# Optimization experiments

Hardware: AMD Instinct MI355X
Metric: run time of the kernel (lower is better)

Reference implementation:

```python
import jax, jax.numpy as jnp
import numpy as np

SCALE_FLOOR = 0.001
N_SOURCES = 16


def setup_inputs() -> dict:
    key = jax.random.key(0)
    ks = jax.random.split(key, 8)
    n, d_in, d = 131072, 1024, 512
    x = jax.random.normal(ks[0], (n, d_in), dtype=jnp.float32)
    source_ids = jax.random.randint(ks[1], (n,), 0, N_SOURCES, dtype=jnp.int64)
    # backbone: single Linear(d_in -> d)
    Wb = jax.random.normal(ks[2], (d_in, d), dtype=jnp.float32) / np.sqrt(d_in)
    bb = jax.random.normal(ks[3], (d,), dtype=jnp.float32) * 0.01
    # pooled head: Linear(d -> 2)
    Wp = jax.random.normal(ks[4], (d, 2), dtype=jnp.float32) / np.sqrt(d)
    bp = jax.random.normal(ks[5], (2,), dtype=jnp.float32) * 0.01
    # per-source heads stacked: [S, d, 2], [S, 2]
    Ws = jax.random.normal(ks[6], (N_SOURCES, d, 2), dtype=jnp.float32) / np.sqrt(d)
    bs = jax.random.normal(ks[7], (N_SOURCES, 2), dtype=jnp.float32) * 0.01
    return {"x": x, "source_ids": source_ids, "Wb": Wb, "bb": bb,
            "Wp": Wp, "bp": bp, "Ws": Ws, "bs": bs}


def _head(raw):
    # raw: (n, 2) -> (mu, scale) with softplus + floor on scale
    mu = raw[:, 0]
    scale = jax.nn.softplus(raw[:, 1]) + SCALE_FLOOR
    return mu, scale


def reference(x, source_ids, Wb, bb, Wp, bp, Ws, bs):
    # backbone embedding: (n, d)
    emb = x @ Wb + bb
    # pooled head
    pooled_mu, pooled_scale = _head(emb @ Wp + bp)
    # routed per-source heads: compute all tiny heads, then gather per row.
    # raw_all: (n, S, 2); S*2 is tiny so this beats gather of per-row weights.
    raw_all = jnp.einsum('nd,sdk->nsk', emb, Ws) + bs[None, :, :]
    raw_sel = jnp.take_along_axis(raw_all, source_ids[:, None, None], axis=1)[:, 0, :]
    src_mu, src_scale = _head(raw_sel)
    # all source ids fall in [0, N_SOURCES), so every row is covered
    # (matches the torch loop where unmatched rows would stay zero).
    return emb, pooled_mu, pooled_scale, src_mu, src_scale
```

## Files before the change

### kernel.cpp

```cpp
#include <hip/hip_runtime.h>

typedef short bf16x8 __attribute__((ext_vector_type(8)));
typedef float f32x4 __attribute__((ext_vector_type(4)));

#define NROWS 131072L
#define DIN 1024
#define DEMB 512
#define NEXT 640

__device__ __forceinline__ unsigned short f2bf(float f) {
  unsigned u = __float_as_uint(f);
  u += 0x7FFFu + ((u >> 16) & 1u);
  return (unsigned short)(u >> 16);
}

__device__ __forceinline__ unsigned pkhi(float a, float b) {
  unsigned ua = __float_as_uint(a) + 0x8000u;
  unsigned ub = __float_as_uint(b) + 0x8000u;
  return __builtin_amdgcn_perm(ub, ua, 0x07060302u);
}

__device__ __forceinline__ float softplusf(float v) {
  return fmaxf(v, 0.f) + log1pf(expf(-fabsf(v)));
}

__global__ __launch_bounds__(256) void wb_transpose(const float* __restrict__ Wb,
                                                    unsigned short* __restrict__ WbT) {
  int g = blockIdx.x * 256 + threadIdx.x;
  int n = g & 511;
  int kb = g >> 9;
  unsigned short tmp[8];
#pragma unroll
  for (int j = 0; j < 8; ++j)
    tmp[j] = f2bf(Wb[(kb * 8 + j) * DEMB + n]);
  uint4 v;
  v.x = (unsigned)tmp[0] | ((unsigned)tmp[1] << 16);
  v.y = (unsigned)tmp[2] | ((unsigned)tmp[3] << 16);
  v.z = (unsigned)tmp[4] | ((unsigned)tmp[5] << 16);
  v.w = (unsigned)tmp[6] | ((unsigned)tmp[7] << 16);
  *(uint4*)(WbT + (long)n * DIN + kb * 8) = v;
}

__global__ void zero_tail(unsigned* __restrict__ p) {
  p[blockIdx.x * 256 + threadIdx.x] = 0u;
}

__global__ __launch_bounds__(256) void wfold_rows(const float* __restrict__ Wb,
                                                  const float* __restrict__ Wp,
                                                  const float* __restrict__ Ws,
                                                  unsigned short* __restrict__ WbT) {
  int w = threadIdx.x >> 6, lane = threadIdx.x & 63;
  int k = blockIdx.x * 4 + w;
  if (lane >= 34) return;
  const float* src;
  if (lane < 2) src = Wp + lane;
  else { int s = (lane - 2) >> 1; src = Ws + s * 1024 + (lane & 1); }
  const float* wrow = Wb + (long)k * DEMB;
  float acc = 0.f;
#pragma unroll 8
  for (int d = 0; d < DEMB; ++d) acc = fmaf(wrow[d], src[2 * d], acc);
  WbT[(long)(512 + lane) * DIN + k] = f2bf(acc);
}

__global__ void bfold_k(const float* __restrict__ bb, const float* __restrict__ Wp,
                        const float* __restrict__ bp, const float* __restrict__ Ws,
                        const float* __restrict__ bs, float* __restrict__ bf) {
  int j = threadIdx.x;
  if (j >= 34) return;
  const float* src; float bias;
  if (j < 2) { src = Wp + j; bias = bp[j]; }
  else { int s = (j - 2) >> 1; src = Ws + s * 1024 + (j & 1); bias = bs[s * 2 + (j & 1)]; }
  float acc = bias;
  for (int d = 0; d < DEMB; ++d) acc = fmaf(bb[d], src[2 * d], acc);
  bf[j] = acc;
}

__global__ __launch_bounds__(256, 3) void gemm_fused(
    const float* __restrict__ x, const unsigned short* __restrict__ wbt,
    const float* __restrict__ bb, const int* __restrict__ sid,
    const float* __restrict__ bfold, float* __restrict__ out) {
  __shared__ unsigned short SM[16384];
  unsigned short* const As0 = SM;
  unsigned short* const As1 = SM + 4096;
  unsigned short* const Bs0 = SM + 8192;
  unsigned short* const Bs1 = SM + 12288;

  const int t = threadIdx.x;
  const int lane = t & 63;
  const int wid = t >> 6;
  const int wm = wid >> 1, wn = wid & 1;

  const int bid = blockIdx.x;
  const int swz = (bid & 7) * 640 + (bid >> 3);
  const int mtile = swz / 5;
  const int ntile = swz - mtile * 5;
  const long m0 = (long)mtile * 128;
  const int n0 = ntile * 128;

  const int arow = t >> 3;
  const int akc = t & 7;
  const int abyte = arow * 64 + ((((akc >> 1) ^ ((t >> 4) & 3)) << 4)) + (akc & 1) * 8;
  const float* xbase = x + (m0 + arow) * DIN + akc * 4;

  const int bn = wid * 16 + (lane >> 2);
  const int bsg = (lane & 3) ^ ((lane >> 3) & 3);
  const unsigned short* bsrc = wbt + (long)(n0 + bn) * DIN + bsg * 8;

  const int l15 = lane & 15, lg = lane >> 4;
  const int kgo = ((lg ^ ((l15 >> 1) & 3)) << 4);
  const int ardrow = (wm * 64 + l15) * 64;
  const int brdrow = (wn * 64 + l15) * 64;

  f32x4 acc[4][4] = {};
  float4 aregA[4], aregB[4];

  auto loadA_A = [&](int k0) {
#pragma unroll
    for (int p = 0; p < 4; ++p)
      aregA[p] = *(const float4*)(xbase + (long)p * 32 * DIN + k0);
  };
  auto loadA_B = [&](int k0) {
#pragma unroll
    for (int p = 0; p < 4; ++p)
      aregB[p] = *(const float4*)(xbase + (long)p * 32 * DIN + k0);
  };
  auto stageB = [&](unsigned short* dst, int k0) {
#pragma unroll
    for (int i = 0; i < 2; ++i) {
      const unsigned short* gp = bsrc + (long)i * 64 * DIN + k0;
      unsigned short* lp = dst + (i * 256 + wid * 64) * 8;
      __builtin_amdgcn_global_load_lds(
          (const __attribute__((address_space(1))) void*)gp,
          (__attribute__((address_space(3))) void*)lp, 16, 0, 0);
    }
  };
  auto writeA_0A = [&]() {
    char* base = (char*)As0;
#pragma unroll
    for (int p = 0; p < 4; ++p) {
      uint2 v; v.x = pkhi(aregA[p].x, aregA[p].y); v.y = pkhi(aregA[p].z, aregA[p].w);
      *(uint2*)(base + abyte + p * 2048) = v;
    }
  };
  auto writeA_1B = [&]() {
    char* base = (char*)As1;
#pragma unroll
    for (int p = 0; p < 4; ++p) {
      uint2 v; v.x = pkhi(aregB[p].x, aregB[p].y); v.y = pkhi(aregB[p].z, aregB[p].w);
      *(uint2*)(base + abyte + p * 2048) = v;
    }
  };
  auto compute = [&](const unsigned short* Au, const unsigned short* Bu) {
    const char* Ab = (const char*)Au;
    const char* Bb = (const char*)Bu;
    bf16x8 af[4], bfv[4];
#pragma unroll
    for (int i = 0; i < 4; ++i) {
      af[i] = *(const bf16x8*)(Ab + ardrow + i * 1024 + kgo);
      bfv[i] = *(const bf16x8*)(Bb + brdrow + i * 1024 + kgo);
    }
#pragma unroll
    for (int mi = 0; mi < 4; ++mi)
#pragma unroll
      for (int ni = 0; ni < 4; ++ni)
        acc[mi][ni] = __builtin_amdgcn_mfma_f32_16x16x32_bf16(af[mi], bfv[ni],
                                                             acc[mi][ni], 0, 0, 0);
  };

  stageB(Bs0, 0);
  loadA_A(0);
  writeA_0A();
  loadA_B(32);
  __builtin_amdgcn_sched_barrier(0);
  asm volatile("s_waitcnt vmcnt(4) lgkmcnt(0)" ::: "memory");
  __builtin_amdgcn_sched_barrier(0);
  __builtin_amdgcn_s_barrier();

#pragma unroll 1
  for (int it = 0; it < 15; ++it) {
    const int ke = it * 2;
    stageB(Bs1, (ke + 1) * 32);
    __builtin_amdgcn_sched_barrier(0);
    loadA_A((ke + 2) * 32);
    compute(As0, Bs0);
    writeA_1B();
    __builtin_amdgcn_sched_barrier(0);
    asm volatile("s_waitcnt vmcnt(4) lgkmcnt(0)" ::: "memory");
    __builtin_amdgcn_sched_barrier(0);
    __builtin_amdgcn_s_barrier();
    stageB(Bs0, (ke + 2) * 32);
    __builtin_amdgcn_sched_barrier(0);
    loadA_B((ke + 3) * 32);
    compute(As1, Bs1);
    writeA_0A();
    __builtin_amdgcn_sched_barrier(0);
    asm volatile("s_waitcnt vmcnt(4) lgkmcnt(0)" ::: "memory");
    __builtin_amdgcn_sched_barrier(0);
    __builtin_amdgcn_s_barrier();
  }

  stageB(Bs1, 31 * 32);
  compute(As0, Bs0);
  writeA_1B();
  __builtin_amdgcn_sched_barrier(0);
  asm volatile("s_waitcnt vmcnt(0) lgkmcnt(0)" ::: "memory");
  __builtin_amdgcn_sched_barrier(0);
  __builtin_amdgcn_s_barrier();
  compute(As1, Bs1);

  if (ntile < 4) {
    const int colg = n0 + wn * 64 + l15;
    float bbv[4];
#pragma unroll
    for (int ni = 0; ni < 4; ++ni) bbv[ni] = bb[colg + ni * 16];
#pragma unroll
    for (int mi = 0; mi < 4; ++mi) {
      const long rbase = m0 + wm * 64 + mi * 16 + lg * 4;
#pragma unroll
      for (int ni = 0; ni < 4; ++ni)
#pragma unroll
        for (int r = 0; r < 4; ++r)
          out[(rbase + r) * DEMB + colg + ni * 16] = acc[mi][ni][r] + bbv[ni];
    }
  } else {
    __syncthreads();
    float* hl = (float*)SM;
    if (wn == 0) {
#pragma unroll
      for (int ni = 0; ni < 3; ++ni)
#pragma unroll
        for (int mi = 0; mi < 4; ++mi)
#pragma unroll
          for (int r = 0; r < 4; ++r) {
            int row = wm * 64 + mi * 16 + lg * 4 + r;
            hl[row * 49 + l15 + ni * 16] = acc[mi][ni][r];
          }
    }
    __syncthreads();
    if (t < 128) {
      const long row = m0 + t;
      const int s = sid[row];
      const float v0 = hl[t * 49 + 0] + bfold[0];
      const float v1 = hl[t * 49 + 1] + bfold[1];
      const float v2 = hl[t * 49 + 2 + 2 * s] + bfold[2 + 2 * s];
      const float v3 = hl[t * 49 + 3 + 2 * s] + bfold[3 + 2 * s];
      float* hp = out + NROWS * DEMB;
      hp[row] = v0;
      hp[NROWS + row] = softplusf(v1) + 0.001f;
      hp[2 * NROWS + row] = v2;
      hp[3 * NROWS + row] = softplusf(v3) + 0.001f;
    }
  }
}

extern "C" void kernel_launch(void* const* d_in, const int* in_sizes, int n_in,
                              void* d_out, int out_size, void* d_ws, size_t ws_size,
                              hipStream_t stream) {
  const float* x  = (const float*)d_in[0];
  const int* sid  = (const int*)d_in[1];
  const float* Wb = (const float*)d_in[2];
  const float* bb = (const float*)d_in[3];
  const float* Wp = (const float*)d_in[4];
  const float* bp = (const float*)d_in[5];
  const float* Ws = (const float*)d_in[6];
  const float* bs = (const float*)d_in[7];
  float* out = (float*)d_out;
  unsigned short* WbT = (unsigned short*)d_ws;
  float* bfoldp = (float*)(WbT + (long)NEXT * DIN);

  wb_transpose<<<256, 256, 0, stream>>>(Wb, WbT);
  zero_tail<<<188, 256, 0, stream>>>((unsigned*)(WbT + 546 * DIN));
  wfold_rows<<<256, 256, 0, stream>>>(Wb, Wp, Ws, WbT);
  bfold_k<<<1, 64, 0, stream>>>(bb, Wp, bp, Ws, bs, bfoldp);
  gemm_fused<<<5120, 256, 0, stream>>>(x, WbT, bb, sid, bfoldp, out);
}
```

Measured before the change: 360.5 us.

## Stream fp32 A tiles straight to LDS via async loads, convert at read

Reads of x no longer go through registers with a bf16 convert-and-store into LDS. fp32 A tiles are now loaded directly into LDS with global_load_lds into a triple-buffered, XOR-swizzled layout, and converted to bf16 when fragments are read for the MFMA. This removes the register staging and LDS write instructions and lets A prefetch run two stages ahead. In exchange LDS use grows to 64KB, launch bounds drop occupancy from 3 to 2 blocks, and each fragment read now needs twice the LDS reads plus pack instructions.

```diff
diff --git a/kernel.cpp b/kernel.cpp
--- a/kernel.cpp
+++ b/kernel.cpp
@@ -2,6 +2,7 @@
 
 typedef short bf16x8 __attribute__((ext_vector_type(8)));
 typedef float f32x4 __attribute__((ext_vector_type(4)));
+typedef unsigned uint4v __attribute__((ext_vector_type(4)));
 
 #define NROWS 131072L
 #define DIN 1024
@@ -75,15 +76,16 @@
   bf[j] = acc;
 }
 
-__global__ __launch_bounds__(256, 3) void gemm_fused(
+__global__ __launch_bounds__(256, 2) void gemm_fused(
     const float* __restrict__ x, const unsigned short* __restrict__ wbt,
     const float* __restrict__ bb, const int* __restrict__ sid,
     const float* __restrict__ bfold, float* __restrict__ out) {
-  __shared__ unsigned short SM[16384];
-  unsigned short* const As0 = SM;
-  unsigned short* const As1 = SM + 4096;
-  unsigned short* const Bs0 = SM + 8192;
-  unsigned short* const Bs1 = SM + 12288;
+  __shared__ __align__(16) char SM[65536];
+  char* const A0 = SM;
+  char* const A1 = SM + 16384;
+  char* const A2 = SM + 32768;
+  char* const B0 = SM + 49152;
+  char* const B1 = SM + 57344;
 
   const int t = threadIdx.x;
   const int lane = t & 63;
@@ -97,67 +99,53 @@
   const long m0 = (long)mtile * 128;
   const int n0 = ntile * 128;
 
-  const int arow = t >> 3;
-  const int akc = t & 7;
-  const int abyte = arow * 64 + ((((akc >> 1) ^ ((t >> 4) & 3)) << 4)) + (akc & 1) * 8;
-  const float* xbase = x + (m0 + arow) * DIN + akc * 4;
+  const int gswA = (t & 7) ^ ((t >> 3) & 7);
+  const float* xA = x + (m0 + (t >> 3)) * DIN + gswA * 4;
 
   const int bn = wid * 16 + (lane >> 2);
   const int bsg = (lane & 3) ^ ((lane >> 3) & 3);
   const unsigned short* bsrc = wbt + (long)(n0 + bn) * DIN + bsg * 8;
 
   const int l15 = lane & 15, lg = lane >> 4;
-  const int kgo = ((lg ^ ((l15 >> 1) & 3)) << 4);
-  const int ardrow = (wm * 64 + l15) * 64;
+  const int kgoB = ((lg ^ ((l15 >> 1) & 3)) << 4);
   const int brdrow = (wn * 64 + l15) * 64;
+  const int arow = (wm * 64 + l15) * 128;
+  const int g0x = (((lg * 2) ^ (l15 & 7)) << 4);
+  const int g1x = (((lg * 2 + 1) ^ (l15 & 7)) << 4);
 
   f32x4 acc[4][4] = {};
-  float4 aregA[4], aregB[4];
-
-  auto loadA_A = [&](int k0) {
-#pragma unroll
-    for (int p = 0; p < 4; ++p)
-      aregA[p] = *(const float4*)(xbase + (long)p * 32 * DIN + k0);
-  };
-  auto loadA_B = [&](int k0) {
-#pragma unroll
-    for (int p = 0; p < 4; ++p)
-      aregB[p] = *(const float4*)(xbase + (long)p * 32 * DIN + k0);
-  };
-  auto stageB = [&](unsigned short* dst, int k0) {
+
+  auto stageA = [&](char* Aw, int k0) {
+#pragma unroll
+    for (int p = 0; p < 4; ++p) {
+      const float* gp = xA + (long)p * 32 * DIN + k0;
+      __builtin_amdgcn_global_load_lds(
+          (const __attribute__((address_space(1))) void*)gp,
+          (__attribute__((address_space(3))) void*)(Aw + p * 4096 + wid * 1024),
+          16, 0, 0);
+    }
+  };
+  auto stageB = [&](char* Bw, int k0) {
 #pragma unroll
     for (int i = 0; i < 2; ++i) {
       const unsigned short* gp = bsrc + (long)i * 64 * DIN + k0;
-      unsigned short* lp = dst + (i * 256 + wid * 64) * 8;
       __builtin_amdgcn_global_load_lds(
           (const __attribute__((address_space(1))) void*)gp,
-          (__attribute__((address_space(3))) void*)lp, 16, 0, 0);
-    }
-  };
-  auto writeA_0A = [&]() {
-    char* base = (char*)As0;
-#pragma unroll
-    for (int p = 0; p < 4; ++p) {
-      uint2 v; v.x = pkhi(aregA[p].x, aregA[p].y); v.y = pkhi(aregA[p].z, aregA[p].w);
-      *(uint2*)(base + abyte + p * 2048) = v;
-    }
-  };
-  auto writeA_1B = [&]() {
-    char* base = (char*)As1;
-#pragma unroll
-    for (int p = 0; p < 4; ++p) {
-      uint2 v; v.x = pkhi(aregB[p].x, aregB[p].y); v.y = pkhi(aregB[p].z, aregB[p].w);
-      *(uint2*)(base + abyte + p * 2048) = v;
-    }
-  };
-  auto compute = [&](const unsigned short* Au, const unsigned short* Bu) {
-    const char* Ab = (const char*)Au;
-    const char* Bb = (const char*)Bu;
+          (__attribute__((address_space(3))) void*)(Bw + i * 4096 + wid * 1024),
+          16, 0, 0);
+    }
+  };
+  auto compute = [&](const char* Ac, const char* Bc) {
     bf16x8 af[4], bfv[4];
 #pragma unroll
     for (int i = 0; i < 4; ++i) {
-      af[i] = *(const bf16x8*)(Ab + ardrow + i * 1024 + kgo);
-      bfv[i] = *(const bf16x8*)(Bb + brdrow + i * 1024 + kgo);
+      f32x4 q0 = *(const f32x4*)(Ac + arow + i * 2048 + g0x);
+      f32x4 q1 = *(const f32x4*)(Ac + arow + i * 2048 + g1x);
+      uint4v u;
+      u[0] = pkhi(q0[0], q0[1]); u[1] = pkhi(q0[2], q0[3]);
+      u[2] = pkhi(q1[0], q1[1]); u[3] = pkhi(q1[2], q1[3]);
+      af[i] = __builtin_bit_cast(bf16x8, u);
+      bfv[i] = *(const bf16x8*)(Bc + brdrow + i * 1024 + kgoB);
     }
 #pragma unroll
     for (int mi = 0; mi < 4; ++mi)
@@ -166,47 +154,40 @@
         acc[mi][ni] = __builtin_amdgcn_mfma_f32_16x16x32_bf16(af[mi], bfv[ni],
                                                              acc[mi][ni], 0, 0, 0);
   };
-
-  stageB(Bs0, 0);
-  loadA_A(0);
-  writeA_0A();
-  loadA_B(32);
-  __builtin_amdgcn_sched_barrier(0);
-  asm volatile("s_waitcnt vmcnt(4) lgkmcnt(0)" ::: "memory");
-  __builtin_amdgcn_sched_barrier(0);
-  __builtin_amdgcn_s_barrier();
-
-#pragma unroll 1
-  for (int it = 0; it < 15; ++it) {
-    const int ke = it * 2;
-    stageB(Bs1, (ke + 1) * 32);
-    __builtin_amdgcn_sched_barrier(0);
-    loadA_A((ke + 2) * 32);
-    compute(As0, Bs0);
-    writeA_1B();
+  auto body = [&](char* Ac, char* Aw, char* Bc, char* Bw, int tt) {
+    stageB(Bw, (tt + 1) * 32);
+    stageA(Aw, (tt + 2) * 32);
+    compute(Ac, Bc);
     __builtin_amdgcn_sched_barrier(0);
     asm volatile("s_waitcnt vmcnt(4) lgkmcnt(0)" ::: "memory");
     __builtin_amdgcn_sched_barrier(0);
     __builtin_amdgcn_s_barrier();
-    stageB(Bs0, (ke + 2) * 32);
-    __builtin_amdgcn_sched_barrier(0);
-    loadA_B((ke + 3) * 32);
-    compute(As1, Bs1);
-    writeA_0A();
-    __builtin_amdgcn_sched_barrier(0);
-    asm volatile("s_waitcnt vmcnt(4) lgkmcnt(0)" ::: "memory");
-    __builtin_amdgcn_sched_barrier(0);
-    __builtin_amdgcn_s_barrier();
+  };
+
+  stageA(A0, 0);
+  stageB(B0, 0);
+  stageA(A1, 32);
+  __builtin_amdgcn_sched_barrier(0);
+  asm volatile("s_waitcnt vmcnt(4) lgkmcnt(0)" ::: "memory");
+  __builtin_amdgcn_sched_barrier(0);
+  __builtin_amdgcn_s_barrier();
+
+#pragma unroll 1
+  for (int tb = 0; tb < 30; tb += 6) {
+    body(A0, A2, B0, B1, tb + 0);
+    body(A1, A0, B1, B0, tb + 1);
+    body(A2, A1, B0, B1, tb + 2);
+    body(A0, A2, B1, B0, tb + 3);
+    body(A1, A0, B0, B1, tb + 4);
+    body(A2, A1, B1, B0, tb + 5);
   }
-
-  stageB(Bs1, 31 * 32);
-  compute(As0, Bs0);
-  writeA_1B();
+  stageB(B1, 31 * 32);
+  compute(A0, B0);
   __builtin_amdgcn_sched_barrier(0);
   asm volatile("s_waitcnt vmcnt(0) lgkmcnt(0)" ::: "memory");
   __builtin_amdgcn_sched_barrier(0);
   __builtin_amdgcn_s_barrier();
-  compute(As1, Bs1);
+  compute(A1, B1);
 
   if (ntile < 4) {
     const int colg = n0 + wn * 64 + l15;
```

New measurement: 366.2 us. About the same (+1.6%).

## Shrink GEMM N-tile to 64 columns to cut padded head work and raise occupancy

Applied to the files above, without the earlier changes.

The fused GEMM tile changes from 128x128 to 128x64. The grid becomes 9 column tiles per row block: 8 for the embedding and 1 for the 34 folded head columns, replacing 5 tiles covering 640 padded columns. This cuts wasted MFMA work on the padded head columns, halves accumulator registers and allows 4 blocks per CU. In exchange, each x row tile is loaded and converted to bf16 nine times instead of five, so activation traffic and conversion VALU work rise. The head epilogue is rewritten for the narrower tile with a 35-float LDS stride.

```diff
diff --git a/kernel.cpp b/kernel.cpp
--- a/kernel.cpp
+++ b/kernel.cpp
@@ -75,15 +75,15 @@
   bf[j] = acc;
 }
 
-__global__ __launch_bounds__(256, 3) void gemm_fused(
+__global__ __launch_bounds__(256, 4) void gemm_fused(
     const float* __restrict__ x, const unsigned short* __restrict__ wbt,
     const float* __restrict__ bb, const int* __restrict__ sid,
     const float* __restrict__ bfold, float* __restrict__ out) {
-  __shared__ unsigned short SM[16384];
-  unsigned short* const As0 = SM;
-  unsigned short* const As1 = SM + 4096;
-  unsigned short* const Bs0 = SM + 8192;
-  unsigned short* const Bs1 = SM + 12288;
+  __shared__ __align__(16) char SM[24576];
+  char* const As0 = SM;
+  char* const As1 = SM + 8192;
+  char* const B0  = SM + 16384;
+  char* const B1  = SM + 20480;
 
   const int t = threadIdx.x;
   const int lane = t & 63;
@@ -91,27 +91,25 @@
   const int wm = wid >> 1, wn = wid & 1;
 
   const int bid = blockIdx.x;
-  const int swz = (bid & 7) * 640 + (bid >> 3);
-  const int mtile = swz / 5;
-  const int ntile = swz - mtile * 5;
+  const int swz = (bid & 7) * 1152 + (bid >> 3);
+  const int mtile = swz / 9;
+  const int ntile = swz - mtile * 9;
   const long m0 = (long)mtile * 128;
-  const int n0 = ntile * 128;
-
-  const int arow = t >> 3;
+  const int n0 = ntile * 64;
+
   const int akc = t & 7;
-  const int abyte = arow * 64 + ((((akc >> 1) ^ ((t >> 4) & 3)) << 4)) + (akc & 1) * 8;
-  const float* xbase = x + (m0 + arow) * DIN + akc * 4;
-
-  const int bn = wid * 16 + (lane >> 2);
-  const int bsg = (lane & 3) ^ ((lane >> 3) & 3);
-  const unsigned short* bsrc = wbt + (long)(n0 + bn) * DIN + bsg * 8;
+  const int abyte = (t >> 3) * 64 + ((((akc >> 1) ^ ((t >> 4) & 3)) << 4)) + (akc & 1) * 8;
+  const float* xbase = x + (m0 + (t >> 3)) * DIN + akc * 4;
+
+  const unsigned short* bsrc =
+      wbt + (long)(n0 + (t >> 2)) * DIN + ((t & 3) ^ ((t >> 3) & 3)) * 8;
 
   const int l15 = lane & 15, lg = lane >> 4;
   const int kgo = ((lg ^ ((l15 >> 1) & 3)) << 4);
   const int ardrow = (wm * 64 + l15) * 64;
-  const int brdrow = (wn * 64 + l15) * 64;
-
-  f32x4 acc[4][4] = {};
+  const int brdrow = (wn * 32 + l15) * 64;
+
+  f32x4 acc[4][2] = {};
   float4 aregA[4], aregB[4];
 
   auto loadA_A = [&](int k0) {
@@ -124,18 +122,15 @@
     for (int p = 0; p < 4; ++p)
       aregB[p] = *(const float4*)(xbase + (long)p * 32 * DIN + k0);
   };
-  auto stageB = [&](unsigned short* dst, int k0) {
-#pragma unroll
-    for (int i = 0; i < 2; ++i) {
-      const unsigned short* gp = bsrc + (long)i * 64 * DIN + k0;
-      unsigned short* lp = dst + (i * 256 + wid * 64) * 8;
-      __builtin_amdgcn_global_load_lds(
-          (const __attribute__((address_space(1))) void*)gp,
-          (__attribute__((address_space(3))) void*)lp, 16, 0, 0);
-    }
+  auto stageB = [&](char* Bw, int k0) {
+    const unsigned short* gp = bsrc + k0;
+    __builtin_amdgcn_global_load_lds(
+        (const __attribute__((address_space(1))) void*)gp,
+        (__attribute__((address_space(3))) void*)(Bw + wid * 1024),
+        16, 0, 0);
   };
   auto writeA_0A = [&]() {
-    char* base = (char*)As0;
+    char* base = As0;
 #pragma unroll
     for (int p = 0; p < 4; ++p) {
       uint2 v; v.x = pkhi(aregA[p].x, aregA[p].y); v.y = pkhi(aregA[p].z, aregA[p].w);
@@ -143,31 +138,30 @@
     }
   };
   auto writeA_1B = [&]() {
-    char* base = (char*)As1;
+    char* base = As1;
 #pragma unroll
     for (int p = 0; p < 4; ++p) {
       uint2 v; v.x = pkhi(aregB[p].x, aregB[p].y); v.y = pkhi(aregB[p].z, aregB[p].w);
       *(uint2*)(base + abyte + p * 2048) = v;
     }
   };
-  auto compute = [&](const unsigned short* Au, const unsigned short* Bu) {
-    const char* Ab = (const char*)Au;
-    const char* Bb = (const char*)Bu;
-    bf16x8 af[4], bfv[4];
-#pragma unroll
-    for (int i = 0; i < 4; ++i) {
+  auto compute = [&](const char* Ab, const char* Bb) {
+    bf16x8 af[4], bfv[2];
+#pragma unroll
+    for (int i = 0; i < 4; ++i)
       af[i] = *(const bf16x8*)(Ab + ardrow + i * 1024 + kgo);
+#pragma unroll
+    for (int i = 0; i < 2; ++i)
       bfv[i] = *(const bf16x8*)(Bb + brdrow + i * 1024 + kgo);
-    }
 #pragma unroll
     for (int mi = 0; mi < 4; ++mi)
 #pragma unroll
-      for (int ni = 0; ni < 4; ++ni)
+      for (int ni = 0; ni < 2; ++ni)
         acc[mi][ni] = __builtin_amdgcn_mfma_f32_16x16x32_bf16(af[mi], bfv[ni],
                                                              acc[mi][ni], 0, 0, 0);
   };
 
-  stageB(Bs0, 0);
+  stageB(B0, 0);
   loadA_A(0);
   writeA_0A();
   loadA_B(32);
@@ -177,47 +171,43 @@
   __builtin_amdgcn_s_barrier();
 
 #pragma unroll 1
-  for (int it = 0; it < 15; ++it) {
-    const int ke = it * 2;
-    stageB(Bs1, (ke + 1) * 32);
-    __builtin_amdgcn_sched_barrier(0);
-    loadA_A((ke + 2) * 32);
-    compute(As0, Bs0);
+  for (int tb = 0; tb < 30; tb += 2) {
+    stageB(B1, (tb + 1) * 32);
+    loadA_A((tb + 2) * 32);
+    compute(As0, B0);
     writeA_1B();
     __builtin_amdgcn_sched_barrier(0);
     asm volatile("s_waitcnt vmcnt(4) lgkmcnt(0)" ::: "memory");
     __builtin_amdgcn_sched_barrier(0);
     __builtin_amdgcn_s_barrier();
-    stageB(Bs0, (ke + 2) * 32);
-    __builtin_amdgcn_sched_barrier(0);
-    loadA_B((ke + 3) * 32);
-    compute(As1, Bs1);
+    stageB(B0, (tb + 2) * 32);
+    loadA_B((tb + 3) * 32);
+    compute(As1, B1);
     writeA_0A();
     __builtin_amdgcn_sched_barrier(0);
     asm volatile("s_waitcnt vmcnt(4) lgkmcnt(0)" ::: "memory");
     __builtin_amdgcn_sched_barrier(0);
     __builtin_amdgcn_s_barrier();
   }
-
-  stageB(Bs1, 31 * 32);
-  compute(As0, Bs0);
+  stageB(B1, 31 * 32);
+  compute(As0, B0);
   writeA_1B();
   __builtin_amdgcn_sched_barrier(0);
   asm volatile("s_waitcnt vmcnt(0) lgkmcnt(0)" ::: "memory");
   __builtin_amdgcn_sched_barrier(0);
   __builtin_amdgcn_s_barrier();
-  compute(As1, Bs1);
-
-  if (ntile < 4) {
-    const int colg = n0 + wn * 64 + l15;
-    float bbv[4];
-#pragma unroll
-    for (int ni = 0; ni < 4; ++ni) bbv[ni] = bb[colg + ni * 16];
+  compute(As1, B1);
+
+  if (ntile < 8) {
+    const int colg = n0 + wn * 32 + l15;
+    float bbv[2];
+#pragma unroll
+    for (int ni = 0; ni < 2; ++ni) bbv[ni] = bb[colg + ni * 16];
 #pragma unroll
     for (int mi = 0; mi < 4; ++mi) {
       const long rbase = m0 + wm * 64 + mi * 16 + lg * 4;
 #pragma unroll
-      for (int ni = 0; ni < 4; ++ni)
+      for (int ni = 0; ni < 2; ++ni)
 #pragma unroll
         for (int r = 0; r < 4; ++r)
           out[(rbase + r) * DEMB + colg + ni * 16] = acc[mi][ni][r] + bbv[ni];
@@ -225,25 +215,29 @@
   } else {
     __syncthreads();
     float* hl = (float*)SM;
-    if (wn == 0) {
-#pragma unroll
-      for (int ni = 0; ni < 3; ++ni)
-#pragma unroll
-        for (int mi = 0; mi < 4; ++mi)
-#pragma unroll
-          for (int r = 0; r < 4; ++r) {
-            int row = wm * 64 + mi * 16 + lg * 4 + r;
-            hl[row * 49 + l15 + ni * 16] = acc[mi][ni][r];
-          }
+    if (wn == 0 || (wn == 1 && l15 < 2)) {
+#pragma unroll
+      for (int ni = 0; ni < 2; ++ni) {
+        int col = wn * 32 + ni * 16 + l15;
+        if (col < 34) {
+#pragma unroll
+          for (int mi = 0; mi < 4; ++mi)
+#pragma unroll
+            for (int r = 0; r < 4; ++r) {
+              int row = wm * 64 + mi * 16 + lg * 4 + r;
+              hl[row * 35 + col] = acc[mi][ni][r];
+            }
+        }
+      }
     }
     __syncthreads();
     if (t < 128) {
       const long row = m0 + t;
       const int s = sid[row];
-      const float v0 = hl[t * 49 + 0] + bfold[0];
-      const float v1 = hl[t * 49 + 1] + bfold[1];
-      const float v2 = hl[t * 49 + 2 + 2 * s] + bfold[2 + 2 * s];
-      const float v3 = hl[t * 49 + 3 + 2 * s] + bfold[3 + 2 * s];
+      const float v0 = hl[t * 35 + 0] + bfold[0];
+      const float v1 = hl[t * 35 + 1] + bfold[1];
+      const float v2 = hl[t * 35 + 2 + 2 * s] + bfold[2 + 2 * s];
+      const float v3 = hl[t * 35 + 3 + 2 * s] + bfold[3 + 2 * s];
       float* hp = out + NROWS * DEMB;
       hp[row] = v0;
       hp[NROWS + row] = softplusf(v1) + 0.001f;
@@ -272,5 +266,5 @@
   zero_tail<<<188, 256, 0, stream>>>((unsigned*)(WbT + 546 * DIN));
   wfold_rows<<<256, 256, 0, stream>>>(Wb, Wp, Ws, WbT);
   bfold_k<<<1, 64, 0, stream>>>(bb, Wp, bp, Ws, bs, bfoldp);
-  gemm_fused<<<5120, 256, 0, stream>>>(x, WbT, bb, sid, bfoldp, out);
-}
+  gemm_fused<<<9216, 256, 0, stream>>>(x, WbT, bb, sid, bfoldp, out);
+}
```

Result: slower. 406.8 us (+12.8%).

## Triple-buffer B tiles with two-deep prefetch and raise MFMA wave priority

Applied to the files above, without the earlier changes.

The GEMM main loop moves from double-buffered B (weight) tiles to three LDS B buffers, so weight tiles are staged two K-steps ahead while x loads stay one step ahead in registers. The loop is unrolled six phases per iteration through a macro, and the waitcnt threshold is relaxed to allow more loads in flight. s_setprio is raised around the MFMA block to favour compute issue. This is meant to hide global-load latency better, at the cost of 40KB of LDS per block instead of 32KB, which may reduce occupancy.

```diff
diff --git a/kernel.cpp b/kernel.cpp
--- a/kernel.cpp
+++ b/kernel.cpp
@@ -79,11 +79,12 @@
     const float* __restrict__ x, const unsigned short* __restrict__ wbt,
     const float* __restrict__ bb, const int* __restrict__ sid,
     const float* __restrict__ bfold, float* __restrict__ out) {
-  __shared__ unsigned short SM[16384];
-  unsigned short* const As0 = SM;
-  unsigned short* const As1 = SM + 4096;
-  unsigned short* const Bs0 = SM + 8192;
-  unsigned short* const Bs1 = SM + 12288;
+  __shared__ __align__(16) char SM[40960];
+  char* const As0 = SM;
+  char* const As1 = SM + 8192;
+  char* const B0  = SM + 16384;
+  char* const B1  = SM + 24576;
+  char* const B2  = SM + 32768;
 
   const int t = threadIdx.x;
   const int lane = t & 63;
@@ -97,10 +98,9 @@
   const long m0 = (long)mtile * 128;
   const int n0 = ntile * 128;
 
-  const int arow = t >> 3;
   const int akc = t & 7;
-  const int abyte = arow * 64 + ((((akc >> 1) ^ ((t >> 4) & 3)) << 4)) + (akc & 1) * 8;
-  const float* xbase = x + (m0 + arow) * DIN + akc * 4;
+  const int abyte = (t >> 3) * 64 + ((((akc >> 1) ^ ((t >> 4) & 3)) << 4)) + (akc & 1) * 8;
+  const float* xbase = x + (m0 + (t >> 3)) * DIN + akc * 4;
 
   const int bn = wid * 16 + (lane >> 2);
   const int bsg = (lane & 3) ^ ((lane >> 3) & 3);
@@ -112,101 +112,97 @@
   const int brdrow = (wn * 64 + l15) * 64;
 
   f32x4 acc[4][4] = {};
-  float4 aregA[4], aregB[4];
-
-  auto loadA_A = [&](int k0) {
+  float4 areg0[4], areg1[4];
+
+  auto loadA0 = [&](int k0) {
 #pragma unroll
     for (int p = 0; p < 4; ++p)
-      aregA[p] = *(const float4*)(xbase + (long)p * 32 * DIN + k0);
-  };
-  auto loadA_B = [&](int k0) {
+      areg0[p] = *(const float4*)(xbase + (long)p * 32 * DIN + k0);
+  };
+  auto loadA1 = [&](int k0) {
 #pragma unroll
     for (int p = 0; p < 4; ++p)
-      aregB[p] = *(const float4*)(xbase + (long)p * 32 * DIN + k0);
-  };
-  auto stageB = [&](unsigned short* dst, int k0) {
+      areg1[p] = *(const float4*)(xbase + (long)p * 32 * DIN + k0);
+  };
+  auto stageB = [&](char* Bw, int k0) {
 #pragma unroll
     for (int i = 0; i < 2; ++i) {
       const unsigned short* gp = bsrc + (long)i * 64 * DIN + k0;
-      unsigned short* lp = dst + (i * 256 + wid * 64) * 8;
       __builtin_amdgcn_global_load_lds(
           (const __attribute__((address_space(1))) void*)gp,
-          (__attribute__((address_space(3))) void*)lp, 16, 0, 0);
-    }
-  };
-  auto writeA_0A = [&]() {
-    char* base = (char*)As0;
+          (__attribute__((address_space(3))) void*)(Bw + i * 4096 + wid * 1024),
+          16, 0, 0);
+    }
+  };
+  auto writeA0 = [&](char* base) {
 #pragma unroll
     for (int p = 0; p < 4; ++p) {
-      uint2 v; v.x = pkhi(aregA[p].x, aregA[p].y); v.y = pkhi(aregA[p].z, aregA[p].w);
+      uint2 v; v.x = pkhi(areg0[p].x, areg0[p].y); v.y = pkhi(areg0[p].z, areg0[p].w);
       *(uint2*)(base + abyte + p * 2048) = v;
     }
   };
-  auto writeA_1B = [&]() {
-    char* base = (char*)As1;
+  auto writeA1 = [&](char* base) {
 #pragma unroll
     for (int p = 0; p < 4; ++p) {
-      uint2 v; v.x = pkhi(aregB[p].x, aregB[p].y); v.y = pkhi(aregB[p].z, aregB[p].w);
+      uint2 v; v.x = pkhi(areg1[p].x, areg1[p].y); v.y = pkhi(areg1[p].z, areg1[p].w);
       *(uint2*)(base + abyte + p * 2048) = v;
     }
   };
-  auto compute = [&](const unsigned short* Au, const unsigned short* Bu) {
-    const char* Ab = (const char*)Au;
-    const char* Bb = (const char*)Bu;
+  auto compute = [&](const char* Ab, const char* Bb) {
     bf16x8 af[4], bfv[4];
 #pragma unroll
     for (int i = 0; i < 4; ++i) {
       af[i] = *(const bf16x8*)(Ab + ardrow + i * 1024 + kgo);
       bfv[i] = *(const bf16x8*)(Bb + brdrow + i * 1024 + kgo);
     }
+    __builtin_amdgcn_s_setprio(1);
 #pragma unroll
     for (int mi = 0; mi < 4; ++mi)
 #pragma unroll
       for (int ni = 0; ni < 4; ++ni)
         acc[mi][ni] = __builtin_amdgcn_mfma_f32_16x16x32_bf16(af[mi], bfv[ni],
                                                              acc[mi][ni], 0, 0, 0);
-  };
-
-  stageB(Bs0, 0);
-  loadA_A(0);
-  writeA_0A();
-  loadA_B(32);
-  __builtin_amdgcn_sched_barrier(0);
-  asm volatile("s_waitcnt vmcnt(4) lgkmcnt(0)" ::: "memory");
-  __builtin_amdgcn_sched_barrier(0);
+    __builtin_amdgcn_s_setprio(0);
+  };
+
+#define PH(BC, BW, AC, AW, LD, WR, TT)                              \
+  stageB(BW, ((TT) + 2) * 32);                                      \
+  LD(((TT) + 2) * 32);                                              \
+  compute(AC, BC);                                                  \
+  WR(AW);                                                           \
+  __builtin_amdgcn_sched_barrier(0);                                \
+  asm volatile("s_waitcnt vmcnt(6) lgkmcnt(0)" ::: "memory");       \
+  __builtin_amdgcn_sched_barrier(0);                                \
   __builtin_amdgcn_s_barrier();
 
+  stageB(B0, 0);
+  loadA0(0);
+  stageB(B1, 32);
+  loadA1(32);
+  writeA0(As0);
+  __builtin_amdgcn_sched_barrier(0);
+  asm volatile("s_waitcnt vmcnt(6) lgkmcnt(0)" ::: "memory");
+  __builtin_amdgcn_sched_barrier(0);
+  __builtin_amdgcn_s_barrier();
+
 #pragma unroll 1
-  for (int it = 0; it < 15; ++it) {
-    const int ke = it * 2;
-    stageB(Bs1, (ke + 1) * 32);
-    __builtin_amdgcn_sched_barrier(0);
-    loadA_A((ke + 2) * 32);
-    compute(As0, Bs0);
-    writeA_1B();
-    __builtin_amdgcn_sched_barrier(0);
-    asm volatile("s_waitcnt vmcnt(4) lgkmcnt(0)" ::: "memory");
-    __builtin_amdgcn_sched_barrier(0);
-    __builtin_amdgcn_s_barrier();
-    stageB(Bs0, (ke + 2) * 32);
-    __builtin_amdgcn_sched_barrier(0);
-    loadA_B((ke + 3) * 32);
-    compute(As1, Bs1);
-    writeA_0A();
-    __builtin_amdgcn_sched_barrier(0);
-    asm volatile("s_waitcnt vmcnt(4) lgkmcnt(0)" ::: "memory");
-    __builtin_amdgcn_sched_barrier(0);
-    __builtin_amdgcn_s_barrier();
+  for (int tb = 0; tb < 30; tb += 6) {
+    PH(B0, B2, As0, As1, loadA0, writeA1, tb + 0)
+    PH(B1, B0, As1, As0, loadA1, writeA0, tb + 1)
+    PH(B2, B1, As0, As1, loadA0, writeA1, tb + 2)
+    PH(B0, B2, As1, As0, loadA1, writeA0, tb + 3)
+    PH(B1, B0, As0, As1, loadA0, writeA1, tb + 4)
+    PH(B2, B1, As1, As0, loadA1, writeA0, tb + 5)
   }
-
-  stageB(Bs1, 31 * 32);
-  compute(As0, Bs0);
-  writeA_1B();
+#undef PH
+
+  compute(As0, B0);
+  writeA1(As1);
   __builtin_amdgcn_sched_barrier(0);
   asm volatile("s_waitcnt vmcnt(0) lgkmcnt(0)" ::: "memory");
   __builtin_amdgcn_sched_barrier(0);
   __builtin_amdgcn_s_barrier();
-  compute(As1, Bs1);
+  compute(As1, B1);
 
   if (ntile < 4) {
     const int colg = n0 + wn * 64 + l15;
```

After: 351.2 us. 1.03x faster.
